# Kernel tuning notes

Hardware: AMD Instinct MI355X
Metric: run time of the kernel (lower is better)

Reference implementation:

```python
import jax, jax.numpy as jnp
import numpy as np

N_EMBD = 1024
N_HEAD = 16
DIM_HEAD = N_EMBD // N_HEAD
# Source code divides scores by scale = dim_head**-0.5, i.e. multiplies by sqrt(dim_head).
INV_SCALE = 1.0 / (DIM_HEAD ** -0.5)


def setup_inputs() -> dict:
    key = jax.random.key(0)
    k1, k2, k3 = jax.random.split(key, 3)
    x = jax.random.normal(k1, (4, 2048, N_EMBD), dtype=jnp.float32)
    # Linear(n_embd, 3*n_embd, bias=False): y = x @ W_qkv  (W stored as [C, 3C])
    W_qkv = jax.random.normal(k2, (N_EMBD, 3 * N_EMBD), dtype=jnp.float32) * (N_EMBD ** -0.5)
    W_proj = jax.random.normal(k3, (N_EMBD, N_EMBD), dtype=jnp.float32) * (N_EMBD ** -0.5)
    return {"x": x, "W_qkv": W_qkv, "W_proj": W_proj}


def reference(x, W_qkv, W_proj):
    B, T, C = x.shape
    qkv = jnp.einsum('btc,cd->btd', x, W_qkv)  # [B,T,3C]
    q, k, v = jnp.split(qkv, 3, axis=-1)
    # [B,T,C] -> [B,H,T,Dh]
    def to_heads(t):
        return t.reshape(B, T, N_HEAD, DIM_HEAD).transpose(0, 2, 1, 3)
    q, k, v = to_heads(q), to_heads(k), to_heads(v)
    scores = jnp.einsum('bhqd,bhkd->bhqk', q, k) * INV_SCALE  # faithful to /scale bug
    causal = jnp.tril(jnp.ones((T, T), dtype=bool))
    scores = jnp.where(causal[None, None], scores, -jnp.inf)
    attn = jax.nn.softmax(scores, axis=-1)
    y = jnp.einsum('bhqk,bhkd->bhqd', attn, v)  # [B,H,T,Dh]
    y = y.transpose(0, 2, 1, 3).reshape(B, T, C)
    return jnp.einsum('btc,cd->btd', y, W_proj)
```

## Files before the change

kernel.cpp:

```cpp
#include <hip/hip_runtime.h>
#include <stdint.h>

typedef unsigned short ushort_t;
typedef __attribute__((ext_vector_type(8))) short short8;
typedef __attribute__((ext_vector_type(8))) _Float16 half8;
typedef __attribute__((ext_vector_type(4))) float f32x4;
typedef __attribute__((ext_vector_type(4))) unsigned short us4;

#define AS1 __attribute__((address_space(1)))
#define AS3 __attribute__((address_space(3)))

#if __has_builtin(__builtin_amdgcn_exp2f)
#define EXP2(x) __builtin_amdgcn_exp2f(x)
#else
#define EXP2(x) exp2f(x)
#endif

#define SC 11.541560327111707f

__device__ __forceinline__ ushort_t f2h(float f) {
  _Float16 h = (_Float16)f;
  return __builtin_bit_cast(unsigned short, h);
}

__device__ __forceinline__ void gload16(const void* g, void* l) {
  __builtin_amdgcn_global_load_lds((AS1 const void*)g, (AS3 void*)l, 16, 0, 0);
}

__device__ __forceinline__ f32x4 mfma16(short8 a, short8 b, f32x4 c) {
  return __builtin_amdgcn_mfma_f32_16x16x32_f16(
      __builtin_bit_cast(half8, a), __builtin_bit_cast(half8, b), c, 0, 0, 0);
}

__global__ __launch_bounds__(256) void cast_f32_f16(const float4* __restrict__ in,
                                                    us4* __restrict__ out, int n4) {
  int i = blockIdx.x * 256 + threadIdx.x;
  int stride = gridDim.x * 256;
  for (; i < n4; i += stride) {
    float4 v = in[i];
    us4 o;
    o[0] = f2h(v.x); o[1] = f2h(v.y); o[2] = f2h(v.z); o[3] = f2h(v.w);
    out[i] = o;
  }
}

__global__ __launch_bounds__(256) void tcast(const float* __restrict__ in,
                                             ushort_t* __restrict__ out, int R, int C) {
  __shared__ __align__(16) float lt[32][33];
  const int r0 = blockIdx.y * 32, c0 = blockIdx.x * 32;
  const int i = threadIdx.x;
  const int lr = i >> 3, lc = (i & 7) * 4;
  float4 v = *(const float4*)(in + (size_t)(r0 + lr) * C + c0 + lc);
  lt[lr][lc + 0] = v.x; lt[lr][lc + 1] = v.y; lt[lr][lc + 2] = v.z; lt[lr][lc + 3] = v.w;
  __syncthreads();
  const int oc = i >> 3;
  const int orr = (i & 7) * 4;
  us4 o;
#pragma unroll
  for (int jj = 0; jj < 4; ++jj) o[jj] = f2h(lt[orr + jj][oc]);
  *(us4*)(out + (size_t)(c0 + oc) * R + r0 + orr) = o;
}

template<int MODE>
__global__ __launch_bounds__(256) void gemm128(
    const ushort_t* __restrict__ A, const ushort_t* __restrict__ Bt, int K, int N,
    ushort_t* __restrict__ qo, ushort_t* __restrict__ ko, ushort_t* __restrict__ vo,
    float* __restrict__ outp)
{
  __shared__ __align__(16) unsigned char lds[32768];
  const int tid = threadIdx.x;
  const int lane = tid & 63, w = tid >> 6;
  const int ln = lane & 15, gq = lane >> 4;
  const int wr = w >> 1, wc = w & 1;
  const int m0 = blockIdx.y * 128, n0 = blockIdx.x * 128;
  const size_t ldb = (size_t)K * 2;
  const unsigned char* ab = (const unsigned char*)A + (size_t)m0 * ldb;
  const unsigned char* bb = (const unsigned char*)Bt + (size_t)n0 * ldb;
  f32x4 acc[4][4] = {};
  const int nkt = K >> 6;
  for (int kb = 0; kb < nkt; ++kb) {
    const unsigned char* abk = ab + kb * 128;
    const unsigned char* bbk = bb + kb * 128;
#pragma unroll
    for (int e = 0; e < 4; ++e) {
      unsigned o = e * 4096 + tid * 16;
      unsigned r = o >> 7;
      unsigned c = (o & 127) ^ ((r & 7) << 4);
      gload16(abk + (size_t)r * ldb + c, lds + o);
      gload16(bbk + (size_t)r * ldb + c, lds + 16384 + o);
    }
    __syncthreads();
    short8 af[4][2], bf8[4][2];
#pragma unroll
    for (int mi = 0; mi < 4; ++mi) {
      unsigned row = wr * 64 + mi * 16 + ln;
      unsigned c0 = (gq * 16) ^ ((row & 7) << 4);
      af[mi][0] = *(const short8*)(lds + row * 128 + c0);
      af[mi][1] = *(const short8*)(lds + row * 128 + (c0 ^ 64));
    }
#pragma unroll
    for (int ni = 0; ni < 4; ++ni) {
      unsigned row = wc * 64 + ni * 16 + ln;
      unsigned c0 = (gq * 16) ^ ((row & 7) << 4);
      bf8[ni][0] = *(const short8*)(lds + 16384 + row * 128 + c0);
      bf8[ni][1] = *(const short8*)(lds + 16384 + row * 128 + (c0 ^ 64));
    }
#pragma unroll
    for (int mi = 0; mi < 4; ++mi)
#pragma unroll
      for (int ni = 0; ni < 4; ++ni) {
        acc[mi][ni] = mfma16(af[mi][0], bf8[ni][0], acc[mi][ni]);
        acc[mi][ni] = mfma16(af[mi][1], bf8[ni][1], acc[mi][ni]);
      }
    __syncthreads();
  }
  if (MODE == 0) {
#pragma unroll
    for (int mi = 0; mi < 4; ++mi)
#pragma unroll
      for (int ni = 0; ni < 4; ++ni)
#pragma unroll
        for (int j = 0; j < 4; ++j) {
          int token = m0 + wr * 64 + mi * 16 + gq * 4 + j;
          int feat  = n0 + wc * 64 + ni * 16 + ln;
          int sec = feat >> 10, cc = feat & 1023;
          int hh = cc >> 6, dd = cc & 63;
          size_t off = (((size_t)(token >> 11) * 16 + hh) * 2048 + (token & 2047)) * 64 + dd;
          ushort_t valb = f2h(acc[mi][ni][j]);
          if (sec == 0) qo[off] = valb;
          else if (sec == 1) ko[off] = valb;
          else vo[off] = valb;
        }
  } else {
#pragma unroll
    for (int mi = 0; mi < 4; ++mi)
#pragma unroll
      for (int ni = 0; ni < 4; ++ni)
#pragma unroll
        for (int j = 0; j < 4; ++j) {
          int token = m0 + wr * 64 + mi * 16 + gq * 4 + j;
          int feat  = n0 + wc * 64 + ni * 16 + ln;
          outp[(size_t)token * N + feat] = acc[mi][ni][j];
        }
  }
}

__global__ __launch_bounds__(256) void transpose_v(const ushort_t* __restrict__ vn,
                                                   ushort_t* __restrict__ vt) {
  __shared__ __align__(16) ushort_t lt[64][80];
  const int bh = blockIdx.y, t0 = blockIdx.x * 64;
  const int i = threadIdx.x;
  {
    const int tr = i >> 2, dc = (i & 3) * 16;
    const ushort_t* src = vn + ((size_t)bh * 2048 + t0 + tr) * 64 + dc;
    *(short8*)&lt[tr][dc] = *(const short8*)src;
    *(short8*)&lt[tr][dc + 8] = *(const short8*)(src + 8);
  }
  __syncthreads();
  {
    const int dr = i >> 2, tc = (i & 3) * 16;
    short8 a, b;
#pragma unroll
    for (int jj = 0; jj < 8; ++jj) a[jj] = (short)lt[tc + jj][dr];
#pragma unroll
    for (int jj = 0; jj < 8; ++jj) b[jj] = (short)lt[tc + 8 + jj][dr];
    ushort_t* dst = vt + ((size_t)bh * 64 + dr) * 2048 + t0 + tc;
    *(short8*)dst = a;
    *(short8*)(dst + 8) = b;
  }
}

__global__ __launch_bounds__(256) void attn_kernel(const ushort_t* __restrict__ qg,
                                                   const ushort_t* __restrict__ kg,
                                                   const ushort_t* __restrict__ vtg,
                                                   ushort_t* __restrict__ yg) {
  __shared__ __align__(16) unsigned char lds[40960];
  const int n = blockIdx.x;
  const int xcd = n & 7, loc = n >> 3;
  const int bh = xcd * 8 + (loc >> 4);
  const int pair = loc & 15;
  const int tid = threadIdx.x;
  const int lane = tid & 63, w = tid >> 6;
  const int ln = lane & 15, gq = lane >> 4;

  const unsigned char* kbase = (const unsigned char*)kg + (size_t)bh * 2048 * 128;
  const unsigned char* vbase = (const unsigned char*)vtg + (size_t)bh * 64 * 4096;
  const ushort_t* qg_bh = qg + (size_t)bh * 2048 * 64;
  const unsigned pw = 32768 + w * 2048;

  auto stage = [&](int buf, int t) {
    const unsigned char* kt = kbase + (size_t)t * 8192;
    const unsigned char* vt = vbase + t * 128;
#pragma unroll
    for (int e = 0; e < 2; ++e) {
      unsigned o = e * 4096 + tid * 16;
      unsigned r = o >> 7;
      unsigned c = (o & 127) ^ ((r & 7) << 4);
      gload16(kt + r * 128 + c, lds + buf * 8192 + o);
      gload16(vt + (size_t)r * 4096 + c, lds + 16384 + buf * 8192 + o);
    }
  };

  int cur = 0;
  for (int ph = 0; ph < 2; ++ph) {
    const int qt = (ph == 0) ? pair : 31 - pair;
    const int q0 = qt * 64;
    const int nt = qt + 1;

    const ushort_t* qrow = qg_bh + (size_t)(q0 + w * 16 + ln) * 64;
    short8 qa0 = *(const short8*)(qrow + gq * 8);
    short8 qa1 = *(const short8*)(qrow + 32 + gq * 8);

    f32x4 yacc[4] = {};
    float mrow = -3e38f, lrow = 0.f;

    stage(cur, 0);
    __syncthreads();

    for (int t = 0; t < nt; ++t) {
      if (t + 1 < nt) stage(cur ^ 1, t + 1);
      const unsigned kb_ = cur * 8192;
      const unsigned vb_ = 16384 + cur * 8192;
      f32x4 s[4];
#pragma unroll
      for (int f = 0; f < 4; ++f) {
        unsigned row = f * 16 + ln;
        unsigned c0 = (gq * 16) ^ ((row & 7) << 4);
        short8 k0 = *(const short8*)(lds + kb_ + row * 128 + c0);
        short8 k1 = *(const short8*)(lds + kb_ + row * 128 + (c0 ^ 64));
        f32x4 z = {0.f, 0.f, 0.f, 0.f};
        z = mfma16(k0, qa0, z);
        s[f] = mfma16(k1, qa1, z);
      }
      if (t == nt - 1) {
        int qloc = w * 16 + ln;
#pragma unroll
        for (int f = 0; f < 4; ++f) {
          int kvb = f * 16 + gq * 4;
#pragma unroll
          for (int j = 0; j < 4; ++j)
            if (kvb + j > qloc) s[f][j] = -3e38f;
        }
      }
      {
        float rm = s[0][0];
#pragma unroll
        for (int f = 0; f < 4; ++f)
#pragma unroll
          for (int j = 0; j < 4; ++j) rm = fmaxf(rm, s[f][j]);
        rm = fmaxf(rm, __shfl_xor(rm, 16));
        rm = fmaxf(rm, __shfl_xor(rm, 32));
        float mnew = fmaxf(mrow, rm);
        float alpha = EXP2((mrow - mnew) * SC);
        float rs = 0.f;
#pragma unroll
        for (int f = 0; f < 4; ++f)
#pragma unroll
          for (int j = 0; j < 4; ++j) {
            float p = EXP2((s[f][j] - mnew) * SC);
            s[f][j] = p;
            rs += p;
          }
        rs += __shfl_xor(rs, 16);
        rs += __shfl_xor(rs, 32);
        lrow = lrow * alpha + rs;
        mrow = mnew;
#pragma unroll
        for (int j = 0; j < 4; ++j) {
          float aj = __shfl(alpha, gq * 4 + j);
#pragma unroll
          for (int df = 0; df < 4; ++df) yacc[df][j] *= aj;
        }
      }
#pragma unroll
      for (int f = 0; f < 4; ++f) {
        us4 pk;
#pragma unroll
        for (int j = 0; j < 4; ++j) pk[j] = f2h(s[f][j]);
        unsigned addr = (pw + ln * 128 + (f * 16 + gq * 4) * 2) ^ ((ln & 7) << 4);
        *(us4*)(lds + addr) = pk;
      }
#pragma unroll
      for (int st = 0; st < 2; ++st) {
        unsigned pc = (st * 64 + gq * 16) ^ ((ln & 7) << 4);
        short8 pa = *(const short8*)(lds + pw + ln * 128 + pc);
#pragma unroll
        for (int df = 0; df < 4; ++df) {
          unsigned row = df * 16 + ln;
          unsigned c0 = (st * 64 + gq * 16) ^ ((row & 7) << 4);
          short8 vb = *(const short8*)(lds + vb_ + row * 128 + c0);
          yacc[df] = mfma16(pa, vb, yacc[df]);
        }
      }
      __syncthreads();
      cur ^= 1;
    }

#pragma unroll
    for (int j = 0; j < 4; ++j) {
      float lj = __shfl(lrow, gq * 4 + j);
      float rl = 1.0f / lj;
      int tq = q0 + w * 16 + gq * 4 + j;
#pragma unroll
      for (int df = 0; df < 4; ++df) {
        int col = (bh & 15) * 64 + df * 16 + ln;
        size_t off = ((size_t)(bh >> 4) * 2048 + tq) * 1024 + col;
        yg[off] = f2h(yacc[df][j] * rl);
      }
    }
  }
}

extern "C" void kernel_launch(void* const* d_in, const int* in_sizes, int n_in,
                              void* d_out, int out_size, void* d_ws, size_t ws_size,
                              hipStream_t stream) {
  (void)in_sizes; (void)n_in; (void)out_size; (void)ws_size;
  const float* x     = (const float*)d_in[0];
  const float* wqkv  = (const float*)d_in[1];
  const float* wproj = (const float*)d_in[2];
  float* out = (float*)d_out;
  char* ws = (char*)d_ws;
  ushort_t* xb   = (ushort_t*)(ws);
  ushort_t* wqkt = (ushort_t*)(ws + 16777216);
  ushort_t* wpt  = (ushort_t*)(ws + 23068672);
  ushort_t* qb_  = (ushort_t*)(ws + 25165824);
  ushort_t* kb_  = (ushort_t*)(ws + 41943040);
  ushort_t* vn   = (ushort_t*)(ws + 58720256);
  ushort_t* vt   = (ushort_t*)(ws + 75497472);
  ushort_t* yb   = xb;

  cast_f32_f16<<<2048, 256, 0, stream>>>((const float4*)x, (us4*)xb, 2097152);
  tcast<<<dim3(96, 32), 256, 0, stream>>>(wqkv, wqkt, 1024, 3072);
  tcast<<<dim3(32, 32), 256, 0, stream>>>(wproj, wpt, 1024, 1024);
  gemm128<0><<<dim3(24, 64), 256, 0, stream>>>(xb, wqkt, 1024, 3072, qb_, kb_, vn, nullptr);
  transpose_v<<<dim3(32, 64), 256, 0, stream>>>(vn, vt);
  attn_kernel<<<1024, 256, 0, stream>>>(qb_, kb_, vt, yb);
  gemm128<1><<<dim3(8, 64), 256, 0, stream>>>(yb, wpt, 1024, 1024, nullptr, nullptr, nullptr, out);
}
```

Measured before the change: 197.0 us.

## Use 128-wide KV tiles and conditional lazy rescale in flash attention

Doubles the KV tile per iteration from 64 to 128 keys, which doubles the LDS buffers to 80KB, halves the loop trip count and halves the barriers and softmax reductions per key. It also skips the online-softmax rescale unless some row max grows by more than a threshold, and folds the scale into a single FMA before exp2. The larger LDS footprint reduces occupancy. Because the KV tile is now wider than the 64-row query tile, diagonal tiles can contain fully masked or wasted key blocks. The lazy rescale lets exponents exceed 1 by up to 2^8, which risks fp16 precision in the P matrix.

```diff
diff --git a/kernel.cpp b/kernel.cpp
--- a/kernel.cpp
+++ b/kernel.cpp
@@ -174,7 +174,7 @@
                                                    const ushort_t* __restrict__ kg,
                                                    const ushort_t* __restrict__ vtg,
                                                    ushort_t* __restrict__ yg) {
-  __shared__ __align__(16) unsigned char lds[40960];
+  __shared__ __align__(16) unsigned char lds[81920];
   const int n = blockIdx.x;
   const int xcd = n & 7, loc = n >> 3;
   const int bh = xcd * 8 + (loc >> 4);
@@ -186,18 +186,24 @@
   const unsigned char* kbase = (const unsigned char*)kg + (size_t)bh * 2048 * 128;
   const unsigned char* vbase = (const unsigned char*)vtg + (size_t)bh * 64 * 4096;
   const ushort_t* qg_bh = qg + (size_t)bh * 2048 * 64;
-  const unsigned pw = 32768 + w * 2048;
-
-  auto stage = [&](int buf, int t) {
-    const unsigned char* kt = kbase + (size_t)t * 8192;
-    const unsigned char* vt = vbase + t * 128;
-#pragma unroll
-    for (int e = 0; e < 2; ++e) {
+  const unsigned pw = 65536 + w * 4096;
+
+  auto stage = [&](int buf, int t2) {
+    const unsigned char* kt = kbase + (size_t)t2 * 16384;
+    const unsigned char* vt = vbase + t2 * 256;
+#pragma unroll
+    for (int e = 0; e < 4; ++e) {
       unsigned o = e * 4096 + tid * 16;
-      unsigned r = o >> 7;
-      unsigned c = (o & 127) ^ ((r & 7) << 4);
-      gload16(kt + r * 128 + c, lds + buf * 8192 + o);
-      gload16(vt + (size_t)r * 4096 + c, lds + 16384 + buf * 8192 + o);
+      {
+        unsigned r = o >> 7;
+        unsigned c = (o & 127) ^ ((r & 7) << 4);
+        gload16(kt + r * 128 + c, lds + buf * 16384 + o);
+      }
+      {
+        unsigned r = o >> 8;
+        unsigned c = (o & 255) ^ ((r & 7) << 4);
+        gload16(vt + (size_t)r * 4096 + c, lds + 32768 + buf * 16384 + o);
+      }
     }
   };
 
@@ -205,7 +211,7 @@
   for (int ph = 0; ph < 2; ++ph) {
     const int qt = (ph == 0) ? pair : 31 - pair;
     const int q0 = qt * 64;
-    const int nt = qt + 1;
+    const int nt2 = (qt + 2) >> 1;
 
     const ushort_t* qrow = qg_bh + (size_t)(q0 + w * 16 + ln) * 64;
     short8 qa0 = *(const short8*)(qrow + gq * 8);
@@ -213,17 +219,18 @@
 
     f32x4 yacc[4] = {};
     float mrow = -3e38f, lrow = 0.f;
+    const int qglob = q0 + w * 16 + ln;
 
     stage(cur, 0);
     __syncthreads();
 
-    for (int t = 0; t < nt; ++t) {
-      if (t + 1 < nt) stage(cur ^ 1, t + 1);
-      const unsigned kb_ = cur * 8192;
-      const unsigned vb_ = 16384 + cur * 8192;
-      f32x4 s[4];
-#pragma unroll
-      for (int f = 0; f < 4; ++f) {
+    for (int t2 = 0; t2 < nt2; ++t2) {
+      if (t2 + 1 < nt2) stage(cur ^ 1, t2 + 1);
+      const unsigned kb_ = cur * 16384;
+      const unsigned vb_ = 32768 + cur * 16384;
+      f32x4 s[8];
+#pragma unroll
+      for (int f = 0; f < 8; ++f) {
         unsigned row = f * 16 + ln;
         unsigned c0 = (gq * 16) ^ ((row & 7) << 4);
         short8 k0 = *(const short8*)(lds + kb_ + row * 128 + c0);
@@ -232,63 +239,67 @@
         z = mfma16(k0, qa0, z);
         s[f] = mfma16(k1, qa1, z);
       }
-      if (t == nt - 1) {
-        int qloc = w * 16 + ln;
-#pragma unroll
-        for (int f = 0; f < 4; ++f) {
-          int kvb = f * 16 + gq * 4;
+      if (t2 == nt2 - 1) {
+        const int kv0 = t2 * 128;
+#pragma unroll
+        for (int f = 0; f < 8; ++f) {
+          int kvb = kv0 + f * 16 + gq * 4;
 #pragma unroll
           for (int j = 0; j < 4; ++j)
-            if (kvb + j > qloc) s[f][j] = -3e38f;
+            if (kvb + j > qglob) s[f][j] = -3e38f;
         }
       }
       {
         float rm = s[0][0];
 #pragma unroll
-        for (int f = 0; f < 4; ++f)
+        for (int f = 0; f < 8; ++f)
 #pragma unroll
           for (int j = 0; j < 4; ++j) rm = fmaxf(rm, s[f][j]);
         rm = fmaxf(rm, __shfl_xor(rm, 16));
         rm = fmaxf(rm, __shfl_xor(rm, 32));
-        float mnew = fmaxf(mrow, rm);
-        float alpha = EXP2((mrow - mnew) * SC);
+        if (__any((rm - mrow) * SC > 8.0f)) {
+          float mnew = fmaxf(mrow, rm);
+          float alpha = EXP2((mrow - mnew) * SC);
+          lrow *= alpha;
+          mrow = mnew;
+#pragma unroll
+          for (int j = 0; j < 4; ++j) {
+            float aj = __shfl(alpha, gq * 4 + j);
+#pragma unroll
+            for (int df = 0; df < 4; ++df) yacc[df][j] *= aj;
+          }
+        }
+        float msc = mrow * SC;
         float rs = 0.f;
 #pragma unroll
-        for (int f = 0; f < 4; ++f)
+        for (int f = 0; f < 8; ++f)
 #pragma unroll
           for (int j = 0; j < 4; ++j) {
-            float p = EXP2((s[f][j] - mnew) * SC);
+            float p = EXP2(__builtin_fmaf(s[f][j], SC, -msc));
             s[f][j] = p;
             rs += p;
           }
         rs += __shfl_xor(rs, 16);
         rs += __shfl_xor(rs, 32);
-        lrow = lrow * alpha + rs;
-        mrow = mnew;
-#pragma unroll
-        for (int j = 0; j < 4; ++j) {
-          float aj = __shfl(alpha, gq * 4 + j);
-#pragma unroll
-          for (int df = 0; df < 4; ++df) yacc[df][j] *= aj;
-        }
-      }
-#pragma unroll
-      for (int f = 0; f < 4; ++f) {
+        lrow += rs;
+      }
+#pragma unroll
+      for (int f = 0; f < 8; ++f) {
         us4 pk;
 #pragma unroll
         for (int j = 0; j < 4; ++j) pk[j] = f2h(s[f][j]);
-        unsigned addr = (pw + ln * 128 + (f * 16 + gq * 4) * 2) ^ ((ln & 7) << 4);
+        unsigned addr = pw + ln * 256 + ((f * 32 + gq * 8) ^ ((ln & 7) << 4));
         *(us4*)(lds + addr) = pk;
       }
 #pragma unroll
-      for (int st = 0; st < 2; ++st) {
+      for (int st = 0; st < 4; ++st) {
         unsigned pc = (st * 64 + gq * 16) ^ ((ln & 7) << 4);
-        short8 pa = *(const short8*)(lds + pw + ln * 128 + pc);
+        short8 pa = *(const short8*)(lds + pw + ln * 256 + pc);
 #pragma unroll
         for (int df = 0; df < 4; ++df) {
           unsigned row = df * 16 + ln;
           unsigned c0 = (st * 64 + gq * 16) ^ ((row & 7) << 4);
-          short8 vb = *(const short8*)(lds + vb_ + row * 128 + c0);
+          short8 vb = *(const short8*)(lds + vb_ + row * 256 + c0);
           yacc[df] = mfma16(pa, vb, yacc[df]);
         }
       }
```

New measurement: 191.4 us. -2.8%, faster.
